# Optimization experiments

Measured on AMD Instinct MI355X. Metric: run time of the kernel, lower is better.

The kernel has to match this reference:

```python
import jax, jax.numpy as jnp
import numpy as np

B, E, NV = 2, 400000, 50000
DE, DV, DC, DOUT = 64, 64, 32, 64
DIN = DE + 2 * DV + DC  # 224


def setup_inputs() -> dict:
    key = jax.random.key(0)
    ks = jax.random.split(key, 7)
    edata = jax.random.normal(ks[0], (B, E, DE), dtype=jnp.float32)
    vdata = jax.random.normal(ks[1], (B, NV, DV), dtype=jnp.float32)
    cdata = jax.random.normal(ks[2], (B, DC), dtype=jnp.float32)
    sender_ids = jax.random.randint(ks[3], (B, E), 0, NV, dtype=jnp.int64)
    receiver_ids = jax.random.randint(ks[4], (B, E), 0, NV, dtype=jnp.int64)
    W = jax.random.normal(ks[5], (DIN, DOUT), dtype=jnp.float32) * (1.0 / np.sqrt(DIN))
    b = jnp.zeros((DOUT,), dtype=jnp.float32)
    return {"edata": edata, "vdata": vdata, "cdata": cdata,
            "sender_ids": sender_ids, "receiver_ids": receiver_ids,
            "W": W, "b": b}


def reference(edata, vdata, cdata, sender_ids, receiver_ids, W, b):
    # gather sender/receiver vertex features: [B,E,DV]
    sender_data = jnp.take_along_axis(vdata, sender_ids[..., None], axis=1)
    receiver_data = jnp.take_along_axis(vdata, receiver_ids[..., None], axis=1)
    # broadcast context per edge: [B,E,DC]
    curr_cdata = jnp.broadcast_to(cdata[:, None, :], (cdata.shape[0], edata.shape[1], cdata.shape[1]))
    # concat along feature dim -> [B,E,DIN], then per-edge-type MLP updater
    etin = jnp.concatenate((edata, sender_data, receiver_data, curr_cdata), axis=2)
    etout = jax.nn.relu(jnp.einsum("bei,io->beo", etin, W) + b)
    return etout
```

## Files before the change

kernel.cpp:

```cpp
#include <hip/hip_runtime.h>
#include <hip/hip_bf16.h>

typedef __bf16 bf16x8 __attribute__((ext_vector_type(8)));
typedef float  f32x4  __attribute__((ext_vector_type(4)));
typedef unsigned short ushort;

#define DE_   64
#define DV_   64
#define DC_   32
#define DOUT_ 64
#define DIN_  224
#define NFRAG 28

__global__ void prep_w_kernel(const float* __restrict__ W, __bf16* __restrict__ wf) {
    int f    = blockIdx.x;
    int lane = threadIdx.x;
    int ks = f >> 2, nt = f & 3;
    int col = nt * 16 + (lane & 15);
    int k0  = ks * 32 + (lane >> 4) * 8;
    bf16x8 v;
#pragma unroll
    for (int j = 0; j < 8; ++j)
        v[j] = (__bf16)W[(k0 + j) * DOUT_ + col];
    reinterpret_cast<bf16x8*>(wf)[f * 64 + lane] = v;
}

__global__ void prep_v_kernel(const float* __restrict__ vdata,
                              __bf16* __restrict__ vb16, int n8) {
    int i = blockIdx.x * blockDim.x + threadIdx.x;
    if (i >= n8) return;
    float4 a = reinterpret_cast<const float4*>(vdata)[2 * i];
    float4 b = reinterpret_cast<const float4*>(vdata)[2 * i + 1];
    bf16x8 v;
    v[0] = (__bf16)a.x; v[1] = (__bf16)a.y; v[2] = (__bf16)a.z; v[3] = (__bf16)a.w;
    v[4] = (__bf16)b.x; v[5] = (__bf16)b.y; v[6] = (__bf16)b.z; v[7] = (__bf16)b.w;
    reinterpret_cast<bf16x8*>(vb16)[i] = v;
}

__global__ __launch_bounds__(1024, 2)
void edge_mlp_kernel(const float* __restrict__ edata,
                     const __bf16* __restrict__ vb16,
                     const float* __restrict__ cdata,
                     const int*   __restrict__ snd,
                     const int*   __restrict__ rcv,
                     const __bf16* __restrict__ wf,
                     const float* __restrict__ bias,
                     float* __restrict__ out,
                     int NV, int n_tiles, int tiles_per_batch) {
    __shared__ bf16x8 wlds[NFRAG * 64];

    const int tid  = threadIdx.x;
    const int lane = tid & 63;
    const int tile = blockIdx.x * (blockDim.x >> 6) + (tid >> 6);
    const bool active = tile < n_tiles;

    const int lr = lane & 15;
    const int lg = lane >> 4;
    const int kl = lg * 8;

    const int  b   = (tile >= tiles_per_batch) ? 1 : 0;
    const long row = active ? ((long)tile * 16 + lr) : 0;

    const int s = snd[row];
    const int r = rcv[row];

    float4 f0[3], f1[3];
#pragma unroll
    for (int ks = 0; ks < 2; ++ks) {
        const float* p = edata + row * DE_ + ks * 32 + kl;
        f0[ks] = *reinterpret_cast<const float4*>(p);
        f1[ks] = *reinterpret_cast<const float4*>(p + 4);
    }
    {
        const float* p = cdata + b * DC_ + kl;
        f0[2] = *reinterpret_cast<const float4*>(p);
        f1[2] = *reinterpret_cast<const float4*>(p + 4);
    }
    float bias_v[4];
#pragma unroll
    for (int nt = 0; nt < 4; ++nt) bias_v[nt] = bias[nt * 16 + lr];

    {
        const bf16x8* wsrc = reinterpret_cast<const bf16x8*>(wf);
        for (int i = tid; i < NFRAG * 64; i += 1024)
            wlds[i] = wsrc[i];
    }
    __syncthreads();

    const __bf16* vbb = vb16 + (long)b * NV * DV_;
    bf16x8 afrag[7];
#pragma unroll
    for (int ks = 2; ks < 6; ++ks) {
        const __bf16* p = (ks < 4) ? (vbb + (long)s * DV_ + (ks - 2) * 32 + kl)
                                   : (vbb + (long)r * DV_ + (ks - 4) * 32 + kl);
        afrag[ks] = *reinterpret_cast<const bf16x8*>(p);
    }
#pragma unroll
    for (int q = 0; q < 3; ++q) {
        int ks = (q < 2) ? q : 6;
        bf16x8 a;
        a[0] = (__bf16)f0[q].x; a[1] = (__bf16)f0[q].y;
        a[2] = (__bf16)f0[q].z; a[3] = (__bf16)f0[q].w;
        a[4] = (__bf16)f1[q].x; a[5] = (__bf16)f1[q].y;
        a[6] = (__bf16)f1[q].z; a[7] = (__bf16)f1[q].w;
        afrag[ks] = a;
    }

    f32x4 acc[4];
#pragma unroll
    for (int nt = 0; nt < 4; ++nt) acc[nt] = f32x4{0.f, 0.f, 0.f, 0.f};

#pragma unroll
    for (int ks = 0; ks < 7; ++ks) {
#pragma unroll
        for (int nt = 0; nt < 4; ++nt) {
            bf16x8 w = wlds[(ks * 4 + nt) * 64 + lane];
            acc[nt] = __builtin_amdgcn_mfma_f32_16x16x32_bf16(afrag[ks], w, acc[nt], 0, 0, 0);
        }
    }

    if (!active) return;

    const long rb = (long)tile * 16;
#pragma unroll
    for (int nt = 0; nt < 4; ++nt) {
#pragma unroll
        for (int j = 0; j < 4; ++j) {
            float v = acc[nt][j] + bias_v[nt];
            out[(rb + lg * 4 + j) * DOUT_ + nt * 16 + lr] = v > 0.f ? v : 0.f;
        }
    }
}

extern "C" void kernel_launch(void* const* d_in, const int* in_sizes, int n_in,
                              void* d_out, int out_size, void* d_ws, size_t ws_size,
                              hipStream_t stream) {
    const float* edata = (const float*)d_in[0];
    const float* vdata = (const float*)d_in[1];
    const float* cdata = (const float*)d_in[2];
    const int*   snd   = (const int*)d_in[3];
    const int*   rcv   = (const int*)d_in[4];
    const float* W     = (const float*)d_in[5];
    const float* bias  = (const float*)d_in[6];
    float* out = (float*)d_out;

    const int Etot = in_sizes[3];
    const int Bb   = in_sizes[2] / DC_;
    const int E    = Etot / Bb;
    const int NV   = in_sizes[1] / (Bb * DV_);
    const int n_tiles = (Etot + 15) / 16;
    const int tiles_per_batch = E / 16;
    const int nvdata = in_sizes[1];

    __bf16* wf   = (__bf16*)d_ws;
    __bf16* vb16 = (__bf16*)((char*)d_ws + NFRAG * 64 * 16);

    hipLaunchKernelGGL(prep_w_kernel, dim3(NFRAG), dim3(64), 0, stream, W, wf);
    {
        int n8 = nvdata / 8;
        hipLaunchKernelGGL(prep_v_kernel, dim3((n8 + 255) / 256), dim3(256), 0,
                           stream, vdata, vb16, n8);
    }

    const int waves_per_block = 16;
    const int blocks = (n_tiles + waves_per_block - 1) / waves_per_block;
    hipLaunchKernelGGL(edge_mlp_kernel, dim3(blocks), dim3(1024), 0, stream,
                       edata, vb16, cdata, snd, rcv, wf, bias, out,
                       NV, n_tiles, tiles_per_batch);
}
```

Measured before the change: 120.9 us.

## Make edge MLP kernel persistent with grid-stride tiles and prefetched indices

The edge MLP kernel now launches a fixed grid of 512 blocks of 1024 threads, and each wave loops over tiles with a grid stride. This loads the weights into LDS once per block instead of once per 16 tiles. The sender and receiver indices for the next tile are fetched during the current tile, so the dependent gather latency overlaps with the current work. The trade-off is fewer resident waves to hide memory latency: each iteration still serialises the vertex gathers and edata loads before the MFMAs, with no deeper pipelining.

```diff
diff --git a/kernel.cpp b/kernel.cpp
--- a/kernel.cpp
+++ b/kernel.cpp
@@ -3,7 +3,6 @@
 
 typedef __bf16 bf16x8 __attribute__((ext_vector_type(8)));
 typedef float  f32x4  __attribute__((ext_vector_type(4)));
-typedef unsigned short ushort;
 
 #define DE_   64
 #define DV_   64
@@ -46,88 +45,99 @@
                      const __bf16* __restrict__ wf,
                      const float* __restrict__ bias,
                      float* __restrict__ out,
-                     int NV, int n_tiles, int tiles_per_batch) {
+                     int NV, int n_tiles, int tiles_per_batch, int total_waves) {
     __shared__ bf16x8 wlds[NFRAG * 64];
 
     const int tid  = threadIdx.x;
     const int lane = tid & 63;
-    const int tile = blockIdx.x * (blockDim.x >> 6) + (tid >> 6);
-    const bool active = tile < n_tiles;
+    const int wid  = blockIdx.x * (blockDim.x >> 6) + (tid >> 6);
 
     const int lr = lane & 15;
     const int lg = lane >> 4;
     const int kl = lg * 8;
-
-    const int  b   = (tile >= tiles_per_batch) ? 1 : 0;
-    const long row = active ? ((long)tile * 16 + lr) : 0;
-
-    const int s = snd[row];
-    const int r = rcv[row];
-
-    float4 f0[3], f1[3];
-#pragma unroll
-    for (int ks = 0; ks < 2; ++ks) {
-        const float* p = edata + row * DE_ + ks * 32 + kl;
-        f0[ks] = *reinterpret_cast<const float4*>(p);
-        f1[ks] = *reinterpret_cast<const float4*>(p + 4);
-    }
-    {
-        const float* p = cdata + b * DC_ + kl;
-        f0[2] = *reinterpret_cast<const float4*>(p);
-        f1[2] = *reinterpret_cast<const float4*>(p + 4);
-    }
-    float bias_v[4];
-#pragma unroll
-    for (int nt = 0; nt < 4; ++nt) bias_v[nt] = bias[nt * 16 + lr];
 
     {
         const bf16x8* wsrc = reinterpret_cast<const bf16x8*>(wf);
         for (int i = tid; i < NFRAG * 64; i += 1024)
             wlds[i] = wsrc[i];
     }
+
+    float bias_v[4];
+#pragma unroll
+    for (int nt = 0; nt < 4; ++nt) bias_v[nt] = bias[nt * 16 + lr];
+
     __syncthreads();
 
-    const __bf16* vbb = vb16 + (long)b * NV * DV_;
-    bf16x8 afrag[7];
-#pragma unroll
-    for (int ks = 2; ks < 6; ++ks) {
-        const __bf16* p = (ks < 4) ? (vbb + (long)s * DV_ + (ks - 2) * 32 + kl)
-                                   : (vbb + (long)r * DV_ + (ks - 4) * 32 + kl);
-        afrag[ks] = *reinterpret_cast<const bf16x8*>(p);
-    }
-#pragma unroll
-    for (int q = 0; q < 3; ++q) {
-        int ks = (q < 2) ? q : 6;
-        bf16x8 a;
-        a[0] = (__bf16)f0[q].x; a[1] = (__bf16)f0[q].y;
-        a[2] = (__bf16)f0[q].z; a[3] = (__bf16)f0[q].w;
-        a[4] = (__bf16)f1[q].x; a[5] = (__bf16)f1[q].y;
-        a[6] = (__bf16)f1[q].z; a[7] = (__bf16)f1[q].w;
-        afrag[ks] = a;
+    int tile = wid;
+    int s = 0, r = 0;
+    if (tile < n_tiles) {
+        long row = (long)tile * 16 + lr;
+        s = snd[row];
+        r = rcv[row];
     }
 
-    f32x4 acc[4];
+    for (; tile < n_tiles; tile += total_waves) {
+        const int  b   = (tile >= tiles_per_batch) ? 1 : 0;
+        const long row = (long)tile * 16 + lr;
+
+        const __bf16* vbb = vb16 + (long)b * NV * DV_;
+        bf16x8 afrag[7];
+        afrag[2] = *reinterpret_cast<const bf16x8*>(vbb + (long)s * DV_ + kl);
+        afrag[3] = *reinterpret_cast<const bf16x8*>(vbb + (long)s * DV_ + 32 + kl);
+        afrag[4] = *reinterpret_cast<const bf16x8*>(vbb + (long)r * DV_ + kl);
+        afrag[5] = *reinterpret_cast<const bf16x8*>(vbb + (long)r * DV_ + 32 + kl);
+
+        const int ntile = tile + total_waves;
+        if (ntile < n_tiles) {
+            long nrow = (long)ntile * 16 + lr;
+            s = snd[nrow];
+            r = rcv[nrow];
+        }
+
+        float4 f0[3], f1[3];
 #pragma unroll
-    for (int nt = 0; nt < 4; ++nt) acc[nt] = f32x4{0.f, 0.f, 0.f, 0.f};
+        for (int ks = 0; ks < 2; ++ks) {
+            const float* p = edata + row * DE_ + ks * 32 + kl;
+            f0[ks] = *reinterpret_cast<const float4*>(p);
+            f1[ks] = *reinterpret_cast<const float4*>(p + 4);
+        }
+        {
+            const float* p = cdata + b * DC_ + kl;
+            f0[2] = *reinterpret_cast<const float4*>(p);
+            f1[2] = *reinterpret_cast<const float4*>(p + 4);
+        }
+#pragma unroll
+        for (int q = 0; q < 3; ++q) {
+            int ks = (q < 2) ? q : 6;
+            bf16x8 a;
+            a[0] = (__bf16)f0[q].x; a[1] = (__bf16)f0[q].y;
+            a[2] = (__bf16)f0[q].z; a[3] = (__bf16)f0[q].w;
+            a[4] = (__bf16)f1[q].x; a[5] = (__bf16)f1[q].y;
+            a[6] = (__bf16)f1[q].z; a[7] = (__bf16)f1[q].w;
+            afrag[ks] = a;
+        }
+
+        f32x4 acc[4];
+#pragma unroll
+        for (int nt = 0; nt < 4; ++nt) acc[nt] = f32x4{0.f, 0.f, 0.f, 0.f};
 
 #pragma unroll
-    for (int ks = 0; ks < 7; ++ks) {
+        for (int ks = 0; ks < 7; ++ks) {
+#pragma unroll
+            for (int nt = 0; nt < 4; ++nt) {
+                bf16x8 w = wlds[(ks * 4 + nt) * 64 + lane];
+                acc[nt] = __builtin_amdgcn_mfma_f32_16x16x32_bf16(afrag[ks], w, acc[nt], 0, 0, 0);
+            }
+        }
+
+        const long rb = (long)tile * 16;
 #pragma unroll
         for (int nt = 0; nt < 4; ++nt) {
-            bf16x8 w = wlds[(ks * 4 + nt) * 64 + lane];
-            acc[nt] = __builtin_amdgcn_mfma_f32_16x16x32_bf16(afrag[ks], w, acc[nt], 0, 0, 0);
-        }
-    }
-
-    if (!active) return;
-
-    const long rb = (long)tile * 16;
 #pragma unroll
-    for (int nt = 0; nt < 4; ++nt) {
-#pragma unroll
-        for (int j = 0; j < 4; ++j) {
-            float v = acc[nt][j] + bias_v[nt];
-            out[(rb + lg * 4 + j) * DOUT_ + nt * 16 + lr] = v > 0.f ? v : 0.f;
+            for (int j = 0; j < 4; ++j) {
+                float v = acc[nt][j] + bias_v[nt];
+                out[(rb + lg * 4 + j) * DOUT_ + nt * 16 + lr] = v > 0.f ? v : 0.f;
+            }
         }
     }
 }
@@ -162,9 +172,10 @@
                            stream, vdata, vb16, n8);
     }
 
+    const int blocks = 512;
     const int waves_per_block = 16;
-    const int blocks = (n_tiles + waves_per_block - 1) / waves_per_block;
+    const int total_waves = blocks * waves_per_block;
     hipLaunchKernelGGL(edge_mlp_kernel, dim3(blocks), dim3(1024), 0, stream,
                        edata, vb16, cdata, snd, rcv, wf, bias, out,
-                       NV, n_tiles, tiles_per_batch);
+                       NV, n_tiles, tiles_per_batch, total_waves);
 }
```

New measurement: 225.5 us. 1.87x slower.
